# Kernel tuning notes

Hardware: AMD Instinct MI355X
Metric: run time of the kernel (lower is better)

The kernel has to match this reference:

```python
import jax, jax.numpy as jnp
import numpy as np

EMB = 128
B = 1024          # number of graphs (segments)
N = 500000        # total nodes
NEG_SLOPE = 0.01  # torch LeakyReLU default


def leaky_relu(v):
    return jnp.where(v >= 0, v, NEG_SLOPE * v)


def setup_inputs() -> dict:
    key = jax.random.key(0)
    ks = jax.random.split(key, 9)
    xg_old = jax.random.normal(ks[0], (B, EMB), dtype=jnp.float32)
    x = jax.random.normal(ks[1], (N, EMB), dtype=jnp.float32)
    batch = jnp.sort(jax.random.randint(ks[2], (N,), 0, B)).astype(jnp.int64)
    s = 1.0 / np.sqrt(EMB)
    w_mask = jax.random.uniform(ks[3], (EMB, 1), jnp.float32, -s, s)
    b_mask = jax.random.uniform(ks[4], (1,), jnp.float32, -s, s)
    w_feat = jax.random.uniform(ks[5], (EMB, EMB), jnp.float32, -s, s)
    b_feat = jax.random.uniform(ks[6], (EMB,), jnp.float32, -s, s)
    s2 = 1.0 / np.sqrt(2 * EMB)
    w_tr = jax.random.uniform(ks[7], (2 * EMB, EMB), jnp.float32, -s2, s2)
    b_tr = jax.random.uniform(ks[8], (EMB,), jnp.float32, -s2, s2)
    return {"xg_old": xg_old, "x": x, "batch": batch,
            "w_mask": w_mask, "b_mask": b_mask,
            "w_feat": w_feat, "b_feat": b_feat,
            "w_tr": w_tr, "b_tr": b_tr}


def reference(xg_old, x, batch, w_mask, b_mask, w_feat, b_feat, w_tr, b_tr):
    batch = batch.astype(jnp.int32)
    # gate score per node, segment-stable softmax over each graph
    gate = (x @ w_mask + b_mask)[:, 0]                        # [N]
    m = jax.ops.segment_max(gate, batch, num_segments=B)      # [B]
    e = jnp.exp(gate - m[batch])                              # [N]
    denom = jax.ops.segment_sum(e, batch, num_segments=B)     # [B]
    alpha = e / denom[batch]                                  # [N]
    # transformed node features, weighted segment-sum pooling
    feat = leaky_relu(x @ w_feat + b_feat)                    # [N, EMB]
    xg = jax.ops.segment_sum(alpha[:, None] * feat, batch, num_segments=B)  # [B, EMB]
    # concat with old global state, linear + LeakyReLU, residual
    cat = jnp.concatenate([xg, xg_old], axis=1)               # [B, 2*EMB]
    out = leaky_relu(cat @ w_tr + b_tr) + xg_old              # [B, EMB]
    return out
```

## Files before the change

### kernel.cpp

```cpp
#include <hip/hip_runtime.h>

typedef __attribute__((ext_vector_type(8))) short short8;
typedef __attribute__((ext_vector_type(4))) float floatx4;

__device__ __forceinline__ float b2f(unsigned int u) { return __uint_as_float(u << 16); }
__device__ __forceinline__ unsigned short f2b(float f) {
    unsigned int u = __float_as_uint(f);
    return (unsigned short)((u + 0x7fffu + ((u >> 16) & 1u)) >> 16);
}
__device__ __forceinline__ unsigned cvtpk(float lo, float hi) {
    unsigned r;
    asm("v_cvt_pk_bf16_f32 %0, %1, %2" : "=v"(r) : "v"(lo), "v"(hi));
    return r;
}
__device__ __forceinline__ void dma16(const void* gsrc, void* ldst) {
    __builtin_amdgcn_global_load_lds(
        (const __attribute__((address_space(1))) void*)gsrc,
        (__attribute__((address_space(3))) void*)ldst, 16, 0, 0);
}

#define EMB 128
#define NN  500000
#define BB  1024
#define NCT 9
#define CH  16
#define WTB (4 * NCT * 512)

__global__ __launch_bounds__(256)
void kinit(float* __restrict__ denom, float* __restrict__ xg,
           unsigned short* __restrict__ wTf, const void* __restrict__ w_feat_,
           const void* __restrict__ w_mask_, const unsigned short* __restrict__ xr,
           const int* __restrict__ braw, int* __restrict__ flags, int N)
{
    __shared__ int sf32;
    int tid = threadIdx.x;
    if (tid < 64) {
        int good = 0;
#pragma unroll
        for (int j = 0; j < 4; ++j) {
            unsigned short u = xr[tid * 4 + j];
            unsigned e = (u >> 7) & 0xffu;
            if ((e >= 100u && e <= 140u) || u == 0) ++good;
        }
#pragma unroll
        for (int o = 1; o < 64; o <<= 1) good += __shfl_xor(good, o);
        if (tid == 0) {
            sf32 = (good < 240) ? 1 : 0;
            if (blockIdx.x == 0) {
                flags[0] = sf32;
                flags[1] = (braw[N - 1] == 0 && braw[N - 2] != 0) ? 1 : 0;
            }
        }
    }
    __syncthreads();
    bool f32 = sf32 != 0;

    int i = blockIdx.x * 256 + tid;
    if (i < BB) denom[i] = 0.f;
    if (i < BB * EMB) xg[i] = 0.f;
    if (i < WTB) {
        int blk = i >> 9, rem = i & 511;
        int lane = rem >> 3, j = rem & 7;
        int kk = blk / NCT, ct = blk - kk * NCT;
        int n = ct * 16 + (lane & 15);
        int k = kk * 32 + (lane >> 4) * 8 + j;
        unsigned short v = 0;
        if (n < 128)      v = f32 ? f2b(((const float*)w_feat_)[k * EMB + n])
                                  : ((const unsigned short*)w_feat_)[k * EMB + n];
        else if (n == 128) v = f32 ? f2b(((const float*)w_mask_)[k])
                                   : ((const unsigned short*)w_mask_)[k];
        wTf[i] = v;
    }
}

__device__ __forceinline__ void flush_racc(float (&racc)[8], int& runSeg,
                                           int quad, int l16, float* __restrict__ xg)
{
    if (runSeg >= 0) {
#pragma unroll
        for (int ct = 0; ct < 8; ++ct) {
            float p = racc[ct];
            p += __shfl_xor(p, 16);
            p += __shfl_xor(p, 32);
            if (quad == (ct & 3))
                atomicAdd(&xg[runSeg * EMB + ct * 16 + l16], p);
            racc[ct] = 0.f;
        }
    }
    runSeg = -1;
}

__device__ __forceinline__ void tile_compute(
    const short8 (&afr)[4], int sv, const unsigned short* __restrict__ lB,
    float bm, const float (&bfv)[8], float* __restrict__ sew,
    int lane, int quad, int l16,
    float* __restrict__ denom, float* __restrict__ xg,
    float (&racc)[8], int& runSeg)
{
    const short8* lBf = (const short8*)lB;
    floatx4 zero = {0.f, 0.f, 0.f, 0.f};
    floatx4 acc[NCT];
#pragma unroll
    for (int ct = 0; ct < NCT; ++ct) acc[ct] = zero;

#pragma unroll
    for (int kk = 0; kk < 4; ++kk)
#pragma unroll
        for (int ct = 0; ct < NCT; ++ct) {
            short8 bf = lBf[(kk * NCT + ct) * 64 + lane];
            acc[ct] = __builtin_amdgcn_mfma_f32_16x16x32_bf16(afr[kk], bf, acc[ct], 0, 0, 0);
        }

    if (l16 == 0) {
#pragma unroll
        for (int r = 0; r < 4; ++r) sew[quad * 4 + r] = acc[8][r];
    }

    float g = sew[l16] + bm;
    float ev = (sv >= 0) ? __expf(fminf(g, 60.f)) : 0.f;

    if (lane < 16) {
        float v = ev;
#pragma unroll
        for (int o = 1; o < 16; o <<= 1) {
            float u  = __shfl_up(v, o);
            int   su = __shfl_up(sv, o);
            if (lane >= o && su == sv) v += u;
        }
        int sn = __shfl_down(sv, 1);
        if (sv >= 0 && (lane == 15 || sn != sv)) atomicAdd(&denom[sv], v);
    }

    float er[4];
#pragma unroll
    for (int r = 0; r < 4; ++r) er[r] = __shfl(ev, quad * 4 + r);

    int sF = __shfl(sv, 0), sL = __shfl(sv, 15);
    if (sF == sL) {
        if (sF >= 0) {
            if (sF != runSeg) { flush_racc(racc, runSeg, quad, l16, xg); runSeg = sF; }
#pragma unroll
            for (int ct = 0; ct < 8; ++ct) {
                float p = 0.f;
#pragma unroll
                for (int r = 0; r < 4; ++r) {
                    float v = acc[ct][r] + bfv[ct];
                    v = v >= 0.f ? v : 0.01f * v;
                    p += v * er[r];
                }
                racc[ct] += p;
            }
        }
    } else {
        flush_racc(racc, runSeg, quad, l16, xg);
        int sr[4];
#pragma unroll
        for (int r = 0; r < 4; ++r) sr[r] = __shfl(sv, quad * 4 + r);
#pragma unroll
        for (int ct = 0; ct < 8; ++ct) {
            int col = ct * 16 + l16;
            float a = 0.f; int cur = -1;
#pragma unroll
            for (int r = 0; r < 4; ++r) {
                int s = sr[r];
                float v = acc[ct][r] + bfv[ct];
                v = v >= 0.f ? v : 0.01f * v;
                v *= er[r];
                if (s != cur) {
                    if (cur >= 0) atomicAdd(&xg[cur * EMB + col], a);
                    a = 0.f; cur = s;
                }
                if (s >= 0) a += v;
            }
            if (cur >= 0) atomicAdd(&xg[cur * EMB + col], a);
        }
    }
}

__global__ __launch_bounds__(256)
void kmain(const void* __restrict__ x_, const int* __restrict__ braw,
           const void* __restrict__ bm_, const void* __restrict__ bf_,
           const unsigned short* __restrict__ wTf, const int* __restrict__ flags,
           float* __restrict__ denom, float* __restrict__ xg, int N)
{
    __shared__ __align__(16) char smem[WTB * 2 + 4 * 16384];
    __shared__ float se[4][16];
    unsigned short* lB = (unsigned short*)smem;

    int tid = threadIdx.x;
    int wave = tid >> 6, lane = tid & 63;
    int quad = lane >> 4, l16 = lane & 15;
    bool f32  = flags[0] != 0;
    bool is64 = flags[1] != 0;

    int T = (N + 15) >> 4;
    int W = blockIdx.x * 4 + wave;
    int t0 = W * CH;
    int tend = t0 + CH; if (tend > T) tend = T;

    {
        const uint4* wg = (const uint4*)wTf;
        uint4* wl = (uint4*)lB;
        uint4 wv[9];
#pragma unroll
        for (int i = 0; i < 9; ++i) wv[i] = wg[i * 256 + tid];
#pragma unroll
        for (int i = 0; i < 9; ++i) wl[i * 256 + tid] = wv[i];
    }
    __syncthreads();
    if (t0 >= tend) return;

    char* xbase = smem + WTB * 2 + wave * 16384;
    const char* xb = (const char*)x_;

    float bm = f32 ? ((const float*)bm_)[0]
                   : b2f((unsigned int)((const unsigned short*)bm_)[0]);
    float bfv[8];
#pragma unroll
    for (int ct = 0; ct < 8; ++ct)
        bfv[ct] = f32 ? ((const float*)bf_)[ct * 16 + l16]
                      : b2f((unsigned int)((const unsigned short*)bf_)[ct * 16 + l16]);

#define DMAF(tt, bufp) do {                                                     \
        int rb_ = (tt) << 4;                                                    \
        _Pragma("unroll")                                                       \
        for (int j = 0; j < 8; ++j) {                                           \
            int r_ = 2 * j + (lane >> 5);                                       \
            unsigned c_ = (unsigned)(((lane & 31) << 4) ^ ((r_ & 7) << 4));     \
            dma16(xb + (((size_t)(rb_ + r_)) << 9) + c_, (bufp) + (j << 10));   \
        }                                                                       \
    } while (0)

#define DMAH(tt, bufp) do {                                                     \
        int rb_ = (tt) << 4;                                                    \
        _Pragma("unroll")                                                       \
        for (int j = 0; j < 4; ++j) {                                           \
            int r_ = 4 * j + (lane >> 4);                                       \
            unsigned c_ = (unsigned)(((lane & 15) << 4) ^ ((r_ & 7) << 4));     \
            dma16(xb + (((size_t)(rb_ + r_)) << 8) + c_, (bufp) + (j << 10));   \
        }                                                                       \
    } while (0)

    if (f32) {
        DMAF(t0, xbase);
        if (t0 + 1 < tend) DMAF(t0 + 1, xbase + 8192);
    } else {
        DMAH(t0, xbase);
        if (t0 + 1 < tend) DMAH(t0 + 1, xbase + 8192);
    }

    float racc[8];
#pragma unroll
    for (int ct = 0; ct < 8; ++ct) racc[ct] = 0.f;
    int runSeg = -1;
    float* sew = se[wave];

    for (int t = t0; t < tend; ++t) {
        char* bufp = xbase + ((t & 1) << 13);

        if (t >= tend - 2) { asm volatile("s_waitcnt vmcnt(0)" ::: "memory"); }
        else if (f32)      { asm volatile("s_waitcnt vmcnt(8)" ::: "memory"); }
        else               { asm volatile("s_waitcnt vmcnt(4)" ::: "memory"); }
        __builtin_amdgcn_sched_barrier(0);

        int n_ = (t << 4) + l16;
        int sv = -1;
        if (n_ < N) { int b_ = is64 ? braw[2 * n_] : braw[n_]; if (b_ >= 0 && b_ < BB) sv = b_; }

        short8 afr[4];
        if (f32) {
            float4 av[8];
#pragma unroll
            for (int kk = 0; kk < 4; ++kk)
#pragma unroll
                for (int h = 0; h < 2; ++h) {
                    unsigned off = (unsigned)(l16 << 9)
                                 + (unsigned)((((kk << 7) + (quad << 5) + (h << 4)) ^ ((l16 & 7) << 4)));
                    av[kk * 2 + h] = *(const float4*)(bufp + off);
                }
#pragma unroll
            for (int kk = 0; kk < 4; ++kk) {
                float4 a = av[kk * 2], b = av[kk * 2 + 1];
                union { short8 s; unsigned u[4]; } cv;
                cv.u[0] = cvtpk(a.x, a.y); cv.u[1] = cvtpk(a.z, a.w);
                cv.u[2] = cvtpk(b.x, b.y); cv.u[3] = cvtpk(b.z, b.w);
                afr[kk] = cv.s;
            }
        } else {
#pragma unroll
            for (int kk = 0; kk < 4; ++kk) {
                unsigned off = (unsigned)(l16 << 8)
                             + (unsigned)((((kk << 6) + (quad << 4)) ^ ((l16 & 7) << 4)));
                afr[kk] = *(const short8*)(bufp + off);
            }
        }

        asm volatile("s_waitcnt lgkmcnt(0)" ::: "memory");
        __builtin_amdgcn_sched_barrier(0);

        if (t + 2 < tend) {
            if (f32) DMAF(t + 2, bufp);
            else     DMAH(t + 2, bufp);
        }

        tile_compute(afr, sv, lB, bm, bfv, sew, lane, quad, l16,
                     denom, xg, racc, runSeg);
    }

    flush_racc(racc, runSeg, quad, l16, xg);
#undef DMAF
#undef DMAH
}

__global__ __launch_bounds__(128)
void kfinal(const float* __restrict__ xg, const float* __restrict__ denom,
            const void* __restrict__ xg_old_, const void* __restrict__ w_tr_,
            const void* __restrict__ b_tr_, const int* __restrict__ flags,
            void* __restrict__ out_)
{
    __shared__ float cat[2 * EMB];
    int b = blockIdx.x, j = threadIdx.x;
    bool f32 = flags[0] != 0;

    float d = denom[b];
    float xgv = xg[b * EMB + j];
    xgv = (d > 0.f) ? xgv / d : 0.f;
    if (xgv != xgv) xgv = 700.0f;
    cat[j] = xgv;
    float old = f32 ? ((const float*)xg_old_)[b * EMB + j]
                    : b2f((unsigned int)((const unsigned short*)xg_old_)[b * EMB + j]);
    cat[EMB + j] = old;
    __syncthreads();

    float acc = f32 ? ((const float*)b_tr_)[j]
                    : b2f((unsigned int)((const unsigned short*)b_tr_)[j]);
    if (f32) {
        const float* w = (const float*)w_tr_;
#pragma unroll 8
        for (int i = 0; i < 2 * EMB; ++i) acc = fmaf(cat[i], w[i * EMB + j], acc);
    } else {
        const unsigned short* w = (const unsigned short*)w_tr_;
#pragma unroll 8
        for (int i = 0; i < 2 * EMB; ++i) acc = fmaf(cat[i], b2f((unsigned int)w[i * EMB + j]), acc);
    }
    acc = acc >= 0.f ? acc : 0.01f * acc;
    acc += old;
    if (acc != acc) acc = 300.0f;

    if (f32) ((float*)out_)[b * EMB + j] = acc;
    else     ((unsigned short*)out_)[b * EMB + j] = f2b(acc);
}

extern "C" void kernel_launch(void* const* d_in, const int* in_sizes, int n_in,
                              void* d_out, int out_size, void* d_ws, size_t ws_size,
                              hipStream_t stream) {
    const void* xg_old = d_in[0];
    const void* x      = d_in[1];
    const int*  braw   = (const int*)d_in[2];
    const void* w_mask = d_in[3];
    const void* b_mask = d_in[4];
    const void* w_feat = d_in[5];
    const void* b_feat = d_in[6];
    const void* w_tr   = d_in[7];
    const void* b_tr   = d_in[8];

    const int N = NN;

    char* ws = (char*)d_ws;
    size_t off = 0;
    int*   flags = (int*)(ws + off);   off += 64;
    float* denom = (float*)(ws + off); off += (size_t)BB * 4;
    float* xg    = (float*)(ws + off); off += (size_t)BB * EMB * 4;
    unsigned short* wTf = (unsigned short*)(ws + off); off += (size_t)WTB * 2;

    int T = (N + 15) >> 4;
    int nblk = (T + 4 * CH - 1) / (4 * CH);
    kinit<<<(BB * EMB + 255) / 256, 256, 0, stream>>>(denom, xg, wTf, w_feat, w_mask,
                                                      (const unsigned short*)x, braw, flags, N);
    kmain<<<nblk, 256, 0, stream>>>(x, braw, b_mask, b_feat, wTf,
                                    flags, denom, xg, N);
    kfinal<<<BB, 128, 0, stream>>>(xg, denom, xg_old, w_tr, b_tr, flags, d_out);
}
```

Before: 397.3 us.

## Hold weight fragments in registers and load x directly, dropping LDS DMA pipeline

Each wave now loads all 36 weight fragments (w_feat and the gate column) into registers instead of staging them in shared memory. x rows are read with plain global vector loads straight into MFMA A-fragments, replacing the double-buffered global_load_lds pipeline. The chunk per wave is halved and launch bounds ask for two blocks per SM. This removes LDS capacity limits and the per-block weight copy, but it uses many registers, loses the explicit prefetch overlap, and doubles the number of blocks that each reload the weights.

```diff
diff --git a/kernel.cpp b/kernel.cpp
--- a/kernel.cpp
+++ b/kernel.cpp
@@ -13,17 +13,12 @@
     asm("v_cvt_pk_bf16_f32 %0, %1, %2" : "=v"(r) : "v"(lo), "v"(hi));
     return r;
 }
-__device__ __forceinline__ void dma16(const void* gsrc, void* ldst) {
-    __builtin_amdgcn_global_load_lds(
-        (const __attribute__((address_space(1))) void*)gsrc,
-        (__attribute__((address_space(3))) void*)ldst, 16, 0, 0);
-}
 
 #define EMB 128
 #define NN  500000
 #define BB  1024
 #define NCT 9
-#define CH  16
+#define CH  8
 #define WTB (4 * NCT * 512)
 
 __global__ __launch_bounds__(256)
@@ -90,102 +85,13 @@
     runSeg = -1;
 }
 
-__device__ __forceinline__ void tile_compute(
-    const short8 (&afr)[4], int sv, const unsigned short* __restrict__ lB,
-    float bm, const float (&bfv)[8], float* __restrict__ sew,
-    int lane, int quad, int l16,
-    float* __restrict__ denom, float* __restrict__ xg,
-    float (&racc)[8], int& runSeg)
-{
-    const short8* lBf = (const short8*)lB;
-    floatx4 zero = {0.f, 0.f, 0.f, 0.f};
-    floatx4 acc[NCT];
-#pragma unroll
-    for (int ct = 0; ct < NCT; ++ct) acc[ct] = zero;
-
-#pragma unroll
-    for (int kk = 0; kk < 4; ++kk)
-#pragma unroll
-        for (int ct = 0; ct < NCT; ++ct) {
-            short8 bf = lBf[(kk * NCT + ct) * 64 + lane];
-            acc[ct] = __builtin_amdgcn_mfma_f32_16x16x32_bf16(afr[kk], bf, acc[ct], 0, 0, 0);
-        }
-
-    if (l16 == 0) {
-#pragma unroll
-        for (int r = 0; r < 4; ++r) sew[quad * 4 + r] = acc[8][r];
-    }
-
-    float g = sew[l16] + bm;
-    float ev = (sv >= 0) ? __expf(fminf(g, 60.f)) : 0.f;
-
-    if (lane < 16) {
-        float v = ev;
-#pragma unroll
-        for (int o = 1; o < 16; o <<= 1) {
-            float u  = __shfl_up(v, o);
-            int   su = __shfl_up(sv, o);
-            if (lane >= o && su == sv) v += u;
-        }
-        int sn = __shfl_down(sv, 1);
-        if (sv >= 0 && (lane == 15 || sn != sv)) atomicAdd(&denom[sv], v);
-    }
-
-    float er[4];
-#pragma unroll
-    for (int r = 0; r < 4; ++r) er[r] = __shfl(ev, quad * 4 + r);
-
-    int sF = __shfl(sv, 0), sL = __shfl(sv, 15);
-    if (sF == sL) {
-        if (sF >= 0) {
-            if (sF != runSeg) { flush_racc(racc, runSeg, quad, l16, xg); runSeg = sF; }
-#pragma unroll
-            for (int ct = 0; ct < 8; ++ct) {
-                float p = 0.f;
-#pragma unroll
-                for (int r = 0; r < 4; ++r) {
-                    float v = acc[ct][r] + bfv[ct];
-                    v = v >= 0.f ? v : 0.01f * v;
-                    p += v * er[r];
-                }
-                racc[ct] += p;
-            }
-        }
-    } else {
-        flush_racc(racc, runSeg, quad, l16, xg);
-        int sr[4];
-#pragma unroll
-        for (int r = 0; r < 4; ++r) sr[r] = __shfl(sv, quad * 4 + r);
-#pragma unroll
-        for (int ct = 0; ct < 8; ++ct) {
-            int col = ct * 16 + l16;
-            float a = 0.f; int cur = -1;
-#pragma unroll
-            for (int r = 0; r < 4; ++r) {
-                int s = sr[r];
-                float v = acc[ct][r] + bfv[ct];
-                v = v >= 0.f ? v : 0.01f * v;
-                v *= er[r];
-                if (s != cur) {
-                    if (cur >= 0) atomicAdd(&xg[cur * EMB + col], a);
-                    a = 0.f; cur = s;
-                }
-                if (s >= 0) a += v;
-            }
-            if (cur >= 0) atomicAdd(&xg[cur * EMB + col], a);
-        }
-    }
-}
-
-__global__ __launch_bounds__(256)
+__global__ __launch_bounds__(256, 2)
 void kmain(const void* __restrict__ x_, const int* __restrict__ braw,
            const void* __restrict__ bm_, const void* __restrict__ bf_,
            const unsigned short* __restrict__ wTf, const int* __restrict__ flags,
            float* __restrict__ denom, float* __restrict__ xg, int N)
 {
-    __shared__ __align__(16) char smem[WTB * 2 + 4 * 16384];
     __shared__ float se[4][16];
-    unsigned short* lB = (unsigned short*)smem;
 
     int tid = threadIdx.x;
     int wave = tid >> 6, lane = tid & 63;
@@ -197,21 +103,14 @@
     int W = blockIdx.x * 4 + wave;
     int t0 = W * CH;
     int tend = t0 + CH; if (tend > T) tend = T;
-
-    {
-        const uint4* wg = (const uint4*)wTf;
-        uint4* wl = (uint4*)lB;
-        uint4 wv[9];
-#pragma unroll
-        for (int i = 0; i < 9; ++i) wv[i] = wg[i * 256 + tid];
-#pragma unroll
-        for (int i = 0; i < 9; ++i) wl[i * 256 + tid] = wv[i];
-    }
-    __syncthreads();
     if (t0 >= tend) return;
 
-    char* xbase = smem + WTB * 2 + wave * 16384;
-    const char* xb = (const char*)x_;
+    short8 bfr[4][NCT];
+#pragma unroll
+    for (int kk = 0; kk < 4; ++kk)
+#pragma unroll
+        for (int ct = 0; ct < NCT; ++ct)
+            bfr[kk][ct] = *(const short8*)(wTf + ((kk * NCT + ct) << 9) + (lane << 3));
 
     float bm = f32 ? ((const float*)bm_)[0]
                    : b2f((unsigned int)((const unsigned short*)bm_)[0]);
@@ -221,33 +120,10 @@
         bfv[ct] = f32 ? ((const float*)bf_)[ct * 16 + l16]
                       : b2f((unsigned int)((const unsigned short*)bf_)[ct * 16 + l16]);
 
-#define DMAF(tt, bufp) do {                                                     \
-        int rb_ = (tt) << 4;                                                    \
-        _Pragma("unroll")                                                       \
-        for (int j = 0; j < 8; ++j) {                                           \
-            int r_ = 2 * j + (lane >> 5);                                       \
-            unsigned c_ = (unsigned)(((lane & 31) << 4) ^ ((r_ & 7) << 4));     \
-            dma16(xb + (((size_t)(rb_ + r_)) << 9) + c_, (bufp) + (j << 10));   \
-        }                                                                       \
-    } while (0)
-
-#define DMAH(tt, bufp) do {                                                     \
-        int rb_ = (tt) << 4;                                                    \
-        _Pragma("unroll")                                                       \
-        for (int j = 0; j < 4; ++j) {                                           \
-            int r_ = 4 * j + (lane >> 4);                                       \
-            unsigned c_ = (unsigned)(((lane & 15) << 4) ^ ((r_ & 7) << 4));     \
-            dma16(xb + (((size_t)(rb_ + r_)) << 8) + c_, (bufp) + (j << 10));   \
-        }                                                                       \
-    } while (0)
-
-    if (f32) {
-        DMAF(t0, xbase);
-        if (t0 + 1 < tend) DMAF(t0 + 1, xbase + 8192);
-    } else {
-        DMAH(t0, xbase);
-        if (t0 + 1 < tend) DMAH(t0 + 1, xbase + 8192);
-    }
+    const float* xf = (const float*)x_;
+    const unsigned short* xu = (const unsigned short*)x_;
+    float4 fz = make_float4(0.f, 0.f, 0.f, 0.f);
+    short8 hz = {0, 0, 0, 0, 0, 0, 0, 0};
 
     float racc[8];
 #pragma unroll
@@ -256,28 +132,20 @@
     float* sew = se[wave];
 
     for (int t = t0; t < tend; ++t) {
-        char* bufp = xbase + ((t & 1) << 13);
-
-        if (t >= tend - 2) { asm volatile("s_waitcnt vmcnt(0)" ::: "memory"); }
-        else if (f32)      { asm volatile("s_waitcnt vmcnt(8)" ::: "memory"); }
-        else               { asm volatile("s_waitcnt vmcnt(4)" ::: "memory"); }
-        __builtin_amdgcn_sched_barrier(0);
-
         int n_ = (t << 4) + l16;
+
         int sv = -1;
         if (n_ < N) { int b_ = is64 ? braw[2 * n_] : braw[n_]; if (b_ >= 0 && b_ < BB) sv = b_; }
 
         short8 afr[4];
         if (f32) {
             float4 av[8];
-#pragma unroll
-            for (int kk = 0; kk < 4; ++kk)
-#pragma unroll
-                for (int h = 0; h < 2; ++h) {
-                    unsigned off = (unsigned)(l16 << 9)
-                                 + (unsigned)((((kk << 7) + (quad << 5) + (h << 4)) ^ ((l16 & 7) << 4)));
-                    av[kk * 2 + h] = *(const float4*)(bufp + off);
-                }
+            const float* p = xf + (size_t)n_ * EMB + quad * 8;
+#pragma unroll
+            for (int kk = 0; kk < 4; ++kk) {
+                av[kk * 2]     = (n_ < N) ? *(const float4*)(p + kk * 32)     : fz;
+                av[kk * 2 + 1] = (n_ < N) ? *(const float4*)(p + kk * 32 + 4) : fz;
+            }
 #pragma unroll
             for (int kk = 0; kk < 4; ++kk) {
                 float4 a = av[kk * 2], b = av[kk * 2 + 1];
@@ -287,29 +155,89 @@
                 afr[kk] = cv.s;
             }
         } else {
-#pragma unroll
-            for (int kk = 0; kk < 4; ++kk) {
-                unsigned off = (unsigned)(l16 << 8)
-                             + (unsigned)((((kk << 6) + (quad << 4)) ^ ((l16 & 7) << 4)));
-                afr[kk] = *(const short8*)(bufp + off);
-            }
-        }
-
-        asm volatile("s_waitcnt lgkmcnt(0)" ::: "memory");
-        __builtin_amdgcn_sched_barrier(0);
-
-        if (t + 2 < tend) {
-            if (f32) DMAF(t + 2, bufp);
-            else     DMAH(t + 2, bufp);
-        }
-
-        tile_compute(afr, sv, lB, bm, bfv, sew, lane, quad, l16,
-                     denom, xg, racc, runSeg);
+            const unsigned short* p = xu + (size_t)n_ * EMB + quad * 8;
+#pragma unroll
+            for (int kk = 0; kk < 4; ++kk)
+                afr[kk] = (n_ < N) ? *(const short8*)(p + kk * 32) : hz;
+        }
+
+        floatx4 zero = {0.f, 0.f, 0.f, 0.f};
+        floatx4 acc[NCT];
+#pragma unroll
+        for (int ct = 0; ct < NCT; ++ct) acc[ct] = zero;
+#pragma unroll
+        for (int kk = 0; kk < 4; ++kk)
+#pragma unroll
+            for (int ct = 0; ct < NCT; ++ct)
+                acc[ct] = __builtin_amdgcn_mfma_f32_16x16x32_bf16(afr[kk], bfr[kk][ct], acc[ct], 0, 0, 0);
+
+        if (l16 == 0) {
+#pragma unroll
+            for (int r = 0; r < 4; ++r) sew[quad * 4 + r] = acc[8][r];
+        }
+
+        float g = sew[l16] + bm;
+        float ev = (sv >= 0) ? __expf(fminf(g, 60.f)) : 0.f;
+
+        if (lane < 16) {
+            float v = ev;
+#pragma unroll
+            for (int o = 1; o < 16; o <<= 1) {
+                float u  = __shfl_up(v, o);
+                int   su = __shfl_up(sv, o);
+                if (lane >= o && su == sv) v += u;
+            }
+            int sn = __shfl_down(sv, 1);
+            if (sv >= 0 && (lane == 15 || sn != sv)) atomicAdd(&denom[sv], v);
+        }
+
+        float er[4];
+#pragma unroll
+        for (int r = 0; r < 4; ++r) er[r] = __shfl(ev, quad * 4 + r);
+
+        int sF = __shfl(sv, 0), sL = __shfl(sv, 15);
+        if (sF == sL) {
+            if (sF >= 0) {
+                if (sF != runSeg) { flush_racc(racc, runSeg, quad, l16, xg); runSeg = sF; }
+#pragma unroll
+                for (int ct = 0; ct < 8; ++ct) {
+                    float p = 0.f;
+#pragma unroll
+                    for (int r = 0; r < 4; ++r) {
+                        float v = acc[ct][r] + bfv[ct];
+                        v = v >= 0.f ? v : 0.01f * v;
+                        p += v * er[r];
+                    }
+                    racc[ct] += p;
+                }
+            }
+        } else {
+            flush_racc(racc, runSeg, quad, l16, xg);
+            int sr[4];
+#pragma unroll
+            for (int r = 0; r < 4; ++r) sr[r] = __shfl(sv, quad * 4 + r);
+#pragma unroll
+            for (int ct = 0; ct < 8; ++ct) {
+                int col = ct * 16 + l16;
+                float a = 0.f; int cur = -1;
+#pragma unroll
+                for (int r = 0; r < 4; ++r) {
+                    int s = sr[r];
+                    float v = acc[ct][r] + bfv[ct];
+                    v = v >= 0.f ? v : 0.01f * v;
+                    v *= er[r];
+                    if (s != cur) {
+                        if (cur >= 0) atomicAdd(&xg[cur * EMB + col], a);
+                        a = 0.f; cur = s;
+                    }
+                    if (s >= 0) a += v;
+                }
+                if (cur >= 0) atomicAdd(&xg[cur * EMB + col], a);
+            }
+        }
     }
 
     flush_racc(racc, runSeg, quad, l16, xg);
-#undef DMAF
-#undef DMAH
 }
 
 __global__ __launch_bounds__(128)
```

Result: slower. 418.3 us (+5.3%).
